# Kernel tuning notes

Measured on AMD Instinct MI355X. Metric: run time of the kernel, lower is better.

The kernel has to match this reference:

```python
import jax, jax.numpy as jnp
from jax import lax
import numpy as np

B, C, H, W = 32, 256, 64, 64
K = 5            # ECA kernel size for C=256
HID = 64         # fusion hidden = C//4
E_LAMBDA = 1e-4


def setup_inputs() -> dict:
    key = jax.random.key(0)
    k1, k2, k3, k4 = jax.random.split(key, 4)
    x = jax.random.normal(k1, (B, C, H, W), dtype=jnp.float32)
    conv_w = jax.random.normal(k2, (1, 1, K), dtype=jnp.float32) * 0.3
    w1 = jax.random.normal(k3, (HID, C), dtype=jnp.float32) * (1.0 / np.sqrt(C))
    w2 = jax.random.normal(k4, (C, HID), dtype=jnp.float32) * (1.0 / np.sqrt(HID))
    return {"x": x, "conv_w": conv_w, "w1": w1, "w2": w2}


def reference(x, conv_w, w1, w2):
    b, c, h, w = x.shape
    # --- shared per-channel mean (used by both ECA's GAP and SimAM) ---
    mean_c = x.mean(axis=(2, 3))                       # [B, C]

    # --- ECA branch: 1D conv over channel dim of GAP, sigmoid gate ---
    y = lax.conv_general_dilated(
        mean_c[:, None, :], conv_w,
        window_strides=(1,), padding=[((K - 1) // 2, (K - 1) // 2)],
        dimension_numbers=("NCH", "OIH", "NCH"))      # [B, 1, C]
    eca_gate = jax.nn.sigmoid(y)[:, 0, :, None, None]  # [B, C, 1, 1]
    x_eca = x * eca_gate

    # --- SimAM branch ---
    n = h * w - 1
    d = x - mean_c[:, :, None, None]                   # [B, C, H, W]
    var = jnp.sum(d * d, axis=(2, 3), keepdims=True) / n
    energy = d * d / (4.0 * (var + E_LAMBDA)) + 0.5
    x_simam = x * jax.nn.sigmoid(energy)

    # --- fusion gate: GAP of (eca+simam) -> 2-layer MLP -> sigmoid ---
    gap = (x_eca + x_simam).mean(axis=(2, 3))          # [B, C]
    hid = jax.nn.relu(gap @ w1.T)                      # [B, HID]
    alpha = jax.nn.sigmoid(hid @ w2.T)[:, :, None, None]  # [B, C, 1, 1]

    return alpha * x_simam + (1.0 - alpha) * x_eca
```

## Files before the change

kernel.cpp:

```cpp
#include <hip/hip_runtime.h>
#include <hip/hip_bf16.h>
#include <math.h>

#define Bdim 32
#define Cdim 256
#define Hdim 64
#define Wdim 64
#define HW   (Hdim * Wdim)
#define KS   5
#define HID  64
#define E_LAMBDA 1e-4f

typedef float vfloat4 __attribute__((ext_vector_type(4)));

__device__ __forceinline__ float sigmoidf(float v) {
    return __builtin_amdgcn_rcpf(1.0f + __expf(-v));
}

__global__ __launch_bounds__(256) void stats_kernel(
        const float* __restrict__ x,
        float* __restrict__ mean_out,
        float* __restrict__ var_out,
        float* __restrict__ ssum_out) {
    const int bc = blockIdx.x;
    const vfloat4* __restrict__ x4 = (const vfloat4*)(x + (size_t)bc * HW);
    const int t = threadIdx.x;

    vfloat4 v[4];
    float sum = 0.0f, sq = 0.0f;
#pragma unroll
    for (int i = 0; i < 4; ++i) {
        v[i] = x4[t + 256 * i];
        sum += v[i].x + v[i].y + v[i].z + v[i].w;
        sq  += v[i].x * v[i].x + v[i].y * v[i].y
             + v[i].z * v[i].z + v[i].w * v[i].w;
    }

#pragma unroll
    for (int off = 32; off > 0; off >>= 1) {
        sum += __shfl_down(sum, off);
        sq  += __shfl_down(sq, off);
    }

    __shared__ float red[8];
    __shared__ float bcast[2];
    const int lane = t & 63;
    const int wid  = t >> 6;
    if (lane == 0) { red[wid] = sum; red[4 + wid] = sq; }
    __syncthreads();
    if (t == 0) {
        const float ts = red[0] + red[1] + red[2] + red[3];
        const float tq = red[4] + red[5] + red[6] + red[7];
        const float mn  = ts * (1.0f / HW);
        const float var = (tq - ts * ts * (1.0f / HW)) * (1.0f / (HW - 1));
        mean_out[bc] = mn;
        var_out[bc]  = var;
        bcast[0] = mn;
        bcast[1] = 0.25f / (var + E_LAMBDA);
    }
    __syncthreads();
    const float mn  = bcast[0];
    const float inv = bcast[1];

    float p = 0.0f;
#pragma unroll
    for (int i = 0; i < 4; ++i) {
        float d;
        d = v[i].x - mn; p += v[i].x * sigmoidf(d * d * inv + 0.5f);
        d = v[i].y - mn; p += v[i].y * sigmoidf(d * d * inv + 0.5f);
        d = v[i].z - mn; p += v[i].z * sigmoidf(d * d * inv + 0.5f);
        d = v[i].w - mn; p += v[i].w * sigmoidf(d * d * inv + 0.5f);
    }
#pragma unroll
    for (int off = 32; off > 0; off >>= 1) p += __shfl_down(p, off);
    if (lane == 0) red[wid] = p;
    __syncthreads();
    if (t == 0) ssum_out[bc] = red[0] + red[1] + red[2] + red[3];
}

__global__ __launch_bounds__(256) void gate_mlp_kernel(
        const float* __restrict__ mean_c,
        const float* __restrict__ ssum,
        const float* __restrict__ conv_w,
        const float* __restrict__ w1,
        const float* __restrict__ w2,
        float* __restrict__ eca_out,
        float* __restrict__ alpha_out) {
    const int b = blockIdx.x;
    const int c = threadIdx.x;
    __shared__ float m[Cdim];
    __shared__ float gap[Cdim];
    __shared__ float hid[HID];

    m[c] = mean_c[b * Cdim + c];
    __syncthreads();

    float acc = 0.0f;
#pragma unroll
    for (int k = 0; k < KS; ++k) {
        const int cc = c + k - (KS - 1) / 2;
        const float mv = (cc >= 0 && cc < Cdim) ? m[cc] : 0.0f;
        acc += conv_w[k] * mv;
    }
    const float gate = sigmoidf(acc);
    eca_out[b * Cdim + c] = gate;
    gap[c] = gate * m[c] + ssum[b * Cdim + c] * (1.0f / HW);
    __syncthreads();

    if (c < HID) {
        float h = 0.0f;
        for (int i = 0; i < Cdim; ++i) h += gap[i] * w1[c * Cdim + i];
        hid[c] = fmaxf(h, 0.0f);
    }
    __syncthreads();

    float a = 0.0f;
#pragma unroll
    for (int j = 0; j < HID; ++j) a += hid[j] * w2[c * HID + j];
    alpha_out[b * Cdim + c] = sigmoidf(a);
}

__global__ __launch_bounds__(256) void final_kernel(
        const float* __restrict__ x,
        const float* __restrict__ mean_c,
        const float* __restrict__ var_c,
        const float* __restrict__ eca,
        const float* __restrict__ alpha,
        float* __restrict__ out) {
    const int bc = blockIdx.x;
    const float mn  = mean_c[bc];
    const float inv = 0.25f / (var_c[bc] + E_LAMBDA);
    const float g   = eca[bc];
    const float a   = alpha[bc];
    const float one_minus_a_g = (1.0f - a) * g;

    const vfloat4* __restrict__ x4 = (const vfloat4*)(x + (size_t)bc * HW);
    vfloat4* __restrict__ o4 = (vfloat4*)(out + (size_t)bc * HW);
    const int t = threadIdx.x;

#pragma unroll
    for (int i = 0; i < 4; ++i) {
        const vfloat4 v = x4[t + 256 * i];
        vfloat4 r;
        float d;
        d = v.x - mn; r.x = v.x * (a * sigmoidf(d * d * inv + 0.5f) + one_minus_a_g);
        d = v.y - mn; r.y = v.y * (a * sigmoidf(d * d * inv + 0.5f) + one_minus_a_g);
        d = v.z - mn; r.z = v.z * (a * sigmoidf(d * d * inv + 0.5f) + one_minus_a_g);
        d = v.w - mn; r.w = v.w * (a * sigmoidf(d * d * inv + 0.5f) + one_minus_a_g);
        __builtin_nontemporal_store(r, &o4[t + 256 * i]);
    }
}

extern "C" void kernel_launch(void* const* d_in, const int* in_sizes, int n_in,
                              void* d_out, int out_size, void* d_ws, size_t ws_size,
                              hipStream_t stream) {
    const float* x      = (const float*)d_in[0];
    const float* conv_w = (const float*)d_in[1];
    const float* w1     = (const float*)d_in[2];
    const float* w2     = (const float*)d_in[3];
    float* out = (float*)d_out;

    const int BC = Bdim * Cdim;
    float* mean_c = (float*)d_ws;
    float* var_c  = mean_c + BC;
    float* ssum   = var_c + BC;
    float* eca    = ssum + BC;
    float* alpha  = eca + BC;

    stats_kernel<<<BC, 256, 0, stream>>>(x, mean_c, var_c, ssum);
    gate_mlp_kernel<<<Bdim, 256, 0, stream>>>(mean_c, ssum, conv_w, w1, w2, eca, alpha);
    final_kernel<<<BC, 256, 0, stream>>>(x, mean_c, var_c, eca, alpha, out);
}
```

Measured before the change: 259.6 us.

## Fuse gate MLP into stats kernel via last-block-per-batch atomic counter

Merges the per-batch ECA conv and fusion MLP into the stats kernel. Each block bumps an atomic counter for its batch, and the last block to finish computes that batch's gate and alpha. This removes one kernel launch and its serialization gap. It adds a memset launch, threadfence/atomic overhead, and stores the precomputed inverse variance so the final kernel skips a division. The MLP dot products are also vectorized with float4 loads.

```diff
diff --git a/kernel.cpp b/kernel.cpp
--- a/kernel.cpp
+++ b/kernel.cpp
@@ -1,5 +1,4 @@
 #include <hip/hip_runtime.h>
-#include <hip/hip_bf16.h>
 #include <math.h>
 
 #define Bdim 32
@@ -17,14 +16,27 @@
     return __builtin_amdgcn_rcpf(1.0f + __expf(-v));
 }
 
-__global__ __launch_bounds__(256) void stats_kernel(
+__global__ __launch_bounds__(256) void stats_gate_kernel(
         const float* __restrict__ x,
+        const float* __restrict__ conv_w,
+        const float* __restrict__ w1,
+        const float* __restrict__ w2,
         float* __restrict__ mean_out,
-        float* __restrict__ var_out,
-        float* __restrict__ ssum_out) {
+        float* __restrict__ inv_out,
+        float* __restrict__ ssum_out,
+        float* __restrict__ gate_out,
+        float* __restrict__ alpha_out,
+        int*   __restrict__ counter) {
     const int bc = blockIdx.x;
+    const int b  = bc >> 8;
     const vfloat4* __restrict__ x4 = (const vfloat4*)(x + (size_t)bc * HW);
     const int t = threadIdx.x;
+    const int lane = t & 63;
+    const int wid  = t >> 6;
+
+    __shared__ float red[8];
+    __shared__ float bcast[2];
+    __shared__ int   slast;
 
     vfloat4 v[4];
     float sum = 0.0f, sq = 0.0f;
@@ -35,17 +47,11 @@
         sq  += v[i].x * v[i].x + v[i].y * v[i].y
              + v[i].z * v[i].z + v[i].w * v[i].w;
     }
-
 #pragma unroll
     for (int off = 32; off > 0; off >>= 1) {
         sum += __shfl_down(sum, off);
         sq  += __shfl_down(sq, off);
     }
-
-    __shared__ float red[8];
-    __shared__ float bcast[2];
-    const int lane = t & 63;
-    const int wid  = t >> 6;
     if (lane == 0) { red[wid] = sum; red[4 + wid] = sq; }
     __syncthreads();
     if (t == 0) {
@@ -54,7 +60,7 @@
         const float mn  = ts * (1.0f / HW);
         const float var = (tq - ts * ts * (1.0f / HW)) * (1.0f / (HW - 1));
         mean_out[bc] = mn;
-        var_out[bc]  = var;
+        inv_out[bc]  = 0.25f / (var + E_LAMBDA);
         bcast[0] = mn;
         bcast[1] = 0.25f / (var + E_LAMBDA);
     }
@@ -75,61 +81,77 @@
     for (int off = 32; off > 0; off >>= 1) p += __shfl_down(p, off);
     if (lane == 0) red[wid] = p;
     __syncthreads();
-    if (t == 0) ssum_out[bc] = red[0] + red[1] + red[2] + red[3];
-}
 
-__global__ __launch_bounds__(256) void gate_mlp_kernel(
-        const float* __restrict__ mean_c,
-        const float* __restrict__ ssum,
-        const float* __restrict__ conv_w,
-        const float* __restrict__ w1,
-        const float* __restrict__ w2,
-        float* __restrict__ eca_out,
-        float* __restrict__ alpha_out) {
-    const int b = blockIdx.x;
-    const int c = threadIdx.x;
-    __shared__ float m[Cdim];
-    __shared__ float gap[Cdim];
-    __shared__ float hid[HID];
+    if (t == 0) {
+        ssum_out[bc] = red[0] + red[1] + red[2] + red[3];
+        __threadfence();
+        const int old = atomicAdd(&counter[b], 1);
+        slast = (old == Cdim - 1);
+    }
+    __syncthreads();
+    if (!slast) return;
 
-    m[c] = mean_c[b * Cdim + c];
+    __threadfence();
+
+    __shared__ float sm[Cdim];
+    __shared__ float sgap[Cdim];
+    __shared__ float shid[HID];
+
+    const float mb = mean_out[b * Cdim + t];
+    const float sb = ssum_out[b * Cdim + t];
+    sm[t] = mb;
     __syncthreads();
 
     float acc = 0.0f;
 #pragma unroll
     for (int k = 0; k < KS; ++k) {
-        const int cc = c + k - (KS - 1) / 2;
-        const float mv = (cc >= 0 && cc < Cdim) ? m[cc] : 0.0f;
+        const int cc = t + k - (KS - 1) / 2;
+        const float mv = (cc >= 0 && cc < Cdim) ? sm[cc] : 0.0f;
         acc += conv_w[k] * mv;
     }
     const float gate = sigmoidf(acc);
-    eca_out[b * Cdim + c] = gate;
-    gap[c] = gate * m[c] + ssum[b * Cdim + c] * (1.0f / HW);
+    gate_out[b * Cdim + t] = gate;
+    sgap[t] = gate * mb + sb * (1.0f / HW);
     __syncthreads();
 
-    if (c < HID) {
+    if (t < HID) {
+        const vfloat4* __restrict__ w14 = (const vfloat4*)(w1 + t * Cdim);
+        const vfloat4* __restrict__ g4  = (const vfloat4*)sgap;
         float h = 0.0f;
-        for (int i = 0; i < Cdim; ++i) h += gap[i] * w1[c * Cdim + i];
-        hid[c] = fmaxf(h, 0.0f);
+#pragma unroll
+        for (int i = 0; i < Cdim / 4; ++i) {
+            const vfloat4 wv = w14[i];
+            const vfloat4 gv = g4[i];
+            h += wv.x * gv.x + wv.y * gv.y + wv.z * gv.z + wv.w * gv.w;
+        }
+        shid[t] = fmaxf(h, 0.0f);
     }
     __syncthreads();
 
-    float a = 0.0f;
+    {
+        const vfloat4* __restrict__ w24 = (const vfloat4*)(w2 + t * HID);
+        const vfloat4* __restrict__ h4  = (const vfloat4*)shid;
+        float a = 0.0f;
 #pragma unroll
-    for (int j = 0; j < HID; ++j) a += hid[j] * w2[c * HID + j];
-    alpha_out[b * Cdim + c] = sigmoidf(a);
+        for (int j = 0; j < HID / 4; ++j) {
+            const vfloat4 wv = w24[j];
+            const vfloat4 hv = h4[j];
+            a += wv.x * hv.x + wv.y * hv.y + wv.z * hv.z + wv.w * hv.w;
+        }
+        alpha_out[b * Cdim + t] = sigmoidf(a);
+    }
 }
 
 __global__ __launch_bounds__(256) void final_kernel(
         const float* __restrict__ x,
         const float* __restrict__ mean_c,
-        const float* __restrict__ var_c,
+        const float* __restrict__ inv_c,
         const float* __restrict__ eca,
         const float* __restrict__ alpha,
         float* __restrict__ out) {
     const int bc = blockIdx.x;
     const float mn  = mean_c[bc];
-    const float inv = 0.25f / (var_c[bc] + E_LAMBDA);
+    const float inv = inv_c[bc];
     const float g   = eca[bc];
     const float a   = alpha[bc];
     const float one_minus_a_g = (1.0f - a) * g;
@@ -162,12 +184,15 @@
 
     const int BC = Bdim * Cdim;
     float* mean_c = (float*)d_ws;
-    float* var_c  = mean_c + BC;
-    float* ssum   = var_c + BC;
+    float* inv_c  = mean_c + BC;
+    float* ssum   = inv_c + BC;
     float* eca    = ssum + BC;
     float* alpha  = eca + BC;
+    int*   cnt    = (int*)(alpha + BC);
 
-    stats_kernel<<<BC, 256, 0, stream>>>(x, mean_c, var_c, ssum);
-    gate_mlp_kernel<<<Bdim, 256, 0, stream>>>(mean_c, ssum, conv_w, w1, w2, eca, alpha);
-    final_kernel<<<BC, 256, 0, stream>>>(x, mean_c, var_c, eca, alpha, out);
+    hipMemsetAsync(cnt, 0, Bdim * sizeof(int), stream);
+
+    stats_gate_kernel<<<BC, 256, 0, stream>>>(x, conv_w, w1, w2,
+                                              mean_c, inv_c, ssum, eca, alpha, cnt);
+    final_kernel<<<BC, 256, 0, stream>>>(x, mean_c, inv_c, eca, alpha, out);
 }
```

Result: slower. 598.0 us (+130.3%).
